# Performance work log

Measured on AMD Instinct MI355X. Metric: run time of the kernel, lower is better.

Reference implementation:

```python
import math
import jax, jax.numpy as jnp
import numpy as np

B, C, D = 4, 1024, 2048
N_EXP, TOP_K, CAP_F = 8, 2, 1.25


def setup_inputs() -> dict:
    key = jax.random.key(0)
    k1, k2, k3, k4 = jax.random.split(key, 4)
    x = jax.random.normal(k1, (B, C, D), dtype=jnp.float32)
    noise = jax.random.normal(k2, (B, C, N_EXP), dtype=jnp.float32)
    w_g = jax.random.normal(k3, (N_EXP, D), dtype=jnp.float32) * 0.02
    w_noise = jax.random.normal(k4, (N_EXP, D), dtype=jnp.float32) * 0.02
    return {"x": x, "noise": noise, "w_g": w_g, "w_noise": w_noise}


def reference(x, noise, w_g, w_noise):
    b, c, d = x.shape
    T = b * c  # num_tokens
    E, k = w_g.shape[0], TOP_K

    # gating logits with noisy top-k (noise eps passed in explicitly)
    logits = jnp.einsum('bcd,ed->bce', x, w_g)
    logits = logits + jax.nn.softplus(jnp.einsum('bcd,ed->bce', x, w_noise)) * noise

    top_vals, top_idx = jax.lax.top_k(logits, k)  # (B,C,k)

    # scatter top-k logits into -inf tensor then softmax == mask non-topk to -inf
    onehot_k = jax.nn.one_hot(top_idx, E, dtype=jnp.int32)  # (B,C,k,E)
    topk_mask = onehot_k.sum(axis=-2) > 0                   # (B,C,E)
    router_probs = jax.nn.softmax(jnp.where(topk_mask, logits, -jnp.inf), axis=-1)

    cap = math.floor(k * CAP_F * T / E)
    cap += cap % 2

    # (k, T, E) expert assignment mask
    exp_mask = onehot_k.reshape(T, k, E).transpose(1, 0, 2)
    # position-in-expert rank via cumulative sum over (k*T, E)
    exp_rank = jnp.cumsum(exp_mask.reshape(k * T, E), axis=0) - 1
    exp_rank = exp_rank.reshape(k, T, E)
    exp_mask = exp_mask * (exp_rank < cap).astype(jnp.int32)
    rank = jnp.sum(exp_mask * exp_rank, axis=-1)  # (k, T) int

    probs_flat = router_probs.reshape(T, E)[None]          # (1,T,E)
    w = exp_mask.astype(x.dtype) * probs_flat              # (k,T,E)
    rank_oh = jax.nn.one_hot(rank, cap, dtype=x.dtype)     # (k,T,cap)
    # combine weights: (T, E, cap)
    exp_weights = jnp.einsum('kte,ktc->tec', w, rank_oh)
    exp_mask_out = exp_weights != 0                        # bool (T,E,cap)

    x_flat = x.reshape(T, d)
    # dense one-hot dispatch matmul: (E, cap, T) @ (T, d)
    expert_batches = jnp.einsum('tec,td->ecd', exp_mask_out.astype(x.dtype), x_flat)
    return exp_weights, exp_mask_out, expert_batches
```

## Files before the change

kernel.cpp:

```cpp
#include <hip/hip_runtime.h>

#define T_TOKENS 4096
#define D_DIM    2048
#define NEXP     8
#define CAP      1280
#define NSLOTS   (NEXP * CAP)

typedef float f32x4 __attribute__((ext_vector_type(4)));

__global__ void gating_kernel(const float* __restrict__ x,
                              const float* __restrict__ noise,
                              const float* __restrict__ w_g,
                              const float* __restrict__ w_noise,
                              int*   __restrict__ top_idx,
                              float* __restrict__ top_prob)
{
    const int wave = threadIdx.x >> 6;
    const int lane = threadIdx.x & 63;
    const int t = blockIdx.x * 4 + wave;
    if (t >= T_TOKENS) return;

    const f32x4* xv = reinterpret_cast<const f32x4*>(x + (size_t)t * D_DIM);

    float acc[16];
#pragma unroll
    for (int j = 0; j < 16; ++j) acc[j] = 0.f;

#pragma unroll
    for (int it = 0; it < 8; ++it) {
        const int c = it * 64 + lane;
        const f32x4 xval = xv[c];
#pragma unroll
        for (int e = 0; e < NEXP; ++e) {
            const f32x4 g = reinterpret_cast<const f32x4*>(w_g + (size_t)e * D_DIM)[c];
            acc[e] += xval.x * g.x + xval.y * g.y + xval.z * g.z + xval.w * g.w;
            const f32x4 n = reinterpret_cast<const f32x4*>(w_noise + (size_t)e * D_DIM)[c];
            acc[8 + e] += xval.x * n.x + xval.y * n.y + xval.z * n.z + xval.w * n.w;
        }
    }

#pragma unroll
    for (int j = 0; j < 16; ++j) {
        float v = acc[j];
#pragma unroll
        for (int off = 32; off > 0; off >>= 1) v += __shfl_down(v, off, 64);
        acc[j] = v;
    }

    if (lane == 0) {
        float logit[NEXP];
#pragma unroll
        for (int e = 0; e < NEXP; ++e) {
            const float z = acc[8 + e];
            const float sp = fmaxf(z, 0.f) + log1pf(expf(-fabsf(z)));
            logit[e] = acc[e] + sp * noise[(size_t)t * NEXP + e];
        }
        int i0 = 0; float v0 = logit[0];
#pragma unroll
        for (int e = 1; e < NEXP; ++e) {
            if (logit[e] > v0) { v0 = logit[e]; i0 = e; }
        }
        int i1 = -1; float v1 = -3.402823466e38f;
#pragma unroll
        for (int e = 0; e < NEXP; ++e) {
            if (e != i0 && logit[e] > v1) { v1 = logit[e]; i1 = e; }
        }
        const float e1  = expf(v1 - v0);
        const float inv = 1.f / (1.f + e1);
        top_idx[t]            = i0;
        top_idx[T_TOKENS + t] = i1;
        top_prob[t]            = inv;
        top_prob[T_TOKENS + t] = e1 * inv;
    }
}

__global__ void scan_kernel(const int* __restrict__ top_idx,
                            int* __restrict__ rank,
                            int* __restrict__ slot_token)
{
    __shared__ int sidx[2 * T_TOKENS];
    __shared__ int scnt[8];

    const int e    = blockIdx.x;
    const int w    = threadIdx.x >> 6;
    const int lane = threadIdx.x & 63;

    for (int i = threadIdx.x; i < 2 * T_TOKENS; i += 512)
        sidx[i] = top_idx[i];
    for (int r = threadIdx.x; r < CAP; r += 512)
        slot_token[e * CAP + r] = -1;
    __syncthreads();

    int cnt = 0;
#pragma unroll
    for (int c = 0; c < 16; ++c) {
        const int i = (w * 16 + c) * 64 + lane;
        cnt += __popcll(__ballot(sidx[i] == e));
    }
    if (lane == 0) scnt[w] = cnt;
    __syncthreads();

    int base = 0;
#pragma unroll
    for (int j = 0; j < 8; ++j) if (j < w) base += scnt[j];

#pragma unroll
    for (int c = 0; c < 16; ++c) {
        const int i = (w * 16 + c) * 64 + lane;
        const bool match = (sidx[i] == e);
        const unsigned long long m = __ballot(match);
        if (match) {
            const int r = base + __popcll(m & ((1ull << lane) - 1ull));
            const bool keep = (r < CAP);
            rank[i] = keep ? r : -1;
            if (keep) slot_token[e * CAP + r] = i;
        }
        base += __popcll(m);
    }
}

__global__ void writer_kernel(const float* __restrict__ x,
                              const int*   __restrict__ top_idx,
                              const float* __restrict__ top_prob,
                              const int*   __restrict__ rank,
                              const int*   __restrict__ slot_token,
                              float* __restrict__ exp_weights,
                              float* __restrict__ exp_mask,
                              float* __restrict__ expert_batches)
{
    const int bid = blockIdx.x;

    if (bid < T_TOKENS) {
        const int t  = bid;
        const int e0 = top_idx[t];
        const int e1 = top_idx[T_TOKENS + t];
        const int r0 = rank[t];
        const int r1 = rank[T_TOKENS + t];
        const float w0 = top_prob[t];
        const float w1 = top_prob[T_TOKENS + t];

        const int p0 = (r0 >= 0) ? (e0 * CAP + r0) : -1;
        const int p1 = (r1 >= 0) ? (e1 * CAP + r1) : -1;
        const float m0 = (w0 != 0.f) ? 1.f : 0.f;
        const float m1 = (w1 != 0.f) ? 1.f : 0.f;

        f32x4* wout = reinterpret_cast<f32x4*>(exp_weights + (size_t)t * NSLOTS);
        f32x4* mout = reinterpret_cast<f32x4*>(exp_mask    + (size_t)t * NSLOTS);

#pragma unroll
        for (int f = threadIdx.x; f < NSLOTS / 4; f += 256) {
            const int b = 4 * f;
            f32x4 wv, mv;
            wv.x = (b     == p0) ? w0 : (b     == p1) ? w1 : 0.f;
            wv.y = (b + 1 == p0) ? w0 : (b + 1 == p1) ? w1 : 0.f;
            wv.z = (b + 2 == p0) ? w0 : (b + 2 == p1) ? w1 : 0.f;
            wv.w = (b + 3 == p0) ? w0 : (b + 3 == p1) ? w1 : 0.f;
            mv.x = (b     == p0) ? m0 : (b     == p1) ? m1 : 0.f;
            mv.y = (b + 1 == p0) ? m0 : (b + 1 == p1) ? m1 : 0.f;
            mv.z = (b + 2 == p0) ? m0 : (b + 2 == p1) ? m1 : 0.f;
            mv.w = (b + 3 == p0) ? m0 : (b + 3 == p1) ? m1 : 0.f;
            __builtin_nontemporal_store(wv, wout + f);
            __builtin_nontemporal_store(mv, mout + f);
        }
    } else {
        const int slot = bid - T_TOKENS;
        const int i = slot_token[slot];
        f32x4* dst = reinterpret_cast<f32x4*>(expert_batches + (size_t)slot * D_DIM);

        if (i >= 0) {
            const int t = i & (T_TOKENS - 1);
            const f32x4* src = reinterpret_cast<const f32x4*>(x + (size_t)t * D_DIM);
#pragma unroll
            for (int c = threadIdx.x; c < D_DIM / 4; c += 256)
                __builtin_nontemporal_store(src[c], dst + c);
        } else {
            const f32x4 z = {0.f, 0.f, 0.f, 0.f};
#pragma unroll
            for (int c = threadIdx.x; c < D_DIM / 4; c += 256)
                __builtin_nontemporal_store(z, dst + c);
        }
    }
}

extern "C" void kernel_launch(void* const* d_in, const int* in_sizes, int n_in,
                              void* d_out, int out_size, void* d_ws, size_t ws_size,
                              hipStream_t stream)
{
    const float* x       = (const float*)d_in[0];
    const float* noise   = (const float*)d_in[1];
    const float* w_g     = (const float*)d_in[2];
    const float* w_noise = (const float*)d_in[3];

    float* out = (float*)d_out;
    const size_t n_ew = (size_t)T_TOKENS * NEXP * CAP;
    float* exp_weights    = out;
    float* exp_mask       = out + n_ew;
    float* expert_batches = out + 2 * n_ew;

    int*   top_idx    = (int*)d_ws;
    float* top_prob   = (float*)((char*)d_ws + 2 * T_TOKENS * 4);
    int*   rank       = (int*)((char*)d_ws + 4 * T_TOKENS * 4);
    int*   slot_token = (int*)((char*)d_ws + 6 * T_TOKENS * 4);

    gating_kernel<<<T_TOKENS / 4, 256, 0, stream>>>(x, noise, w_g, w_noise,
                                                    top_idx, top_prob);
    scan_kernel<<<NEXP, 512, 0, stream>>>(top_idx, rank, slot_token);
    writer_kernel<<<T_TOKENS + NSLOTS, 256, 0, stream>>>(x, top_idx, top_prob,
                                                         rank, slot_token,
                                                         exp_weights, exp_mask,
                                                         expert_batches);
}
```

Baseline: 121.2 us.

## Overlap zero-fill of weight/mask outputs with gating and scatter nonzeros in scan

The dense zero fill of exp_weights and exp_mask moves into extra blocks of the gating kernel, so it runs alongside the gating matmul. The scan kernel then scatters the few nonzero weight and mask entries directly, which removes the per-token writer pass and its compare-and-select work. The final kernel now only copies expert batches. The cost is a stricter ordering: the scatter relies on the fill having finished first, which holds because the kernels run in order on one stream, and the scatter stores are uncoalesced.

Measured after the change: 119.0 us. About the same (-1.8%).

```diff
diff --git a/kernel.cpp b/kernel.cpp
--- a/kernel.cpp
+++ b/kernel.cpp
@@ -6,19 +6,35 @@
 #define CAP      1280
 #define NSLOTS   (NEXP * CAP)
 
+#define GATE_BLOCKS (T_TOKENS / 4)
+#define FILL_FLOATS (2ull * T_TOKENS * NSLOTS)
+#define FILL_VEC_PER_BLOCK 4096
+#define FILL_BLOCKS (FILL_FLOATS / (4 * FILL_VEC_PER_BLOCK))
+
 typedef float f32x4 __attribute__((ext_vector_type(4)));
 
-__global__ void gating_kernel(const float* __restrict__ x,
-                              const float* __restrict__ noise,
-                              const float* __restrict__ w_g,
-                              const float* __restrict__ w_noise,
-                              int*   __restrict__ top_idx,
-                              float* __restrict__ top_prob)
+__global__ void gate_fill_kernel(const float* __restrict__ x,
+                                 const float* __restrict__ noise,
+                                 const float* __restrict__ w_g,
+                                 const float* __restrict__ w_noise,
+                                 int*   __restrict__ top_idx,
+                                 float* __restrict__ top_prob,
+                                 float* __restrict__ wm_base)
 {
+    if (blockIdx.x >= GATE_BLOCKS) {
+        const size_t blk = blockIdx.x - GATE_BLOCKS;
+        f32x4* dst = reinterpret_cast<f32x4*>(wm_base) + blk * FILL_VEC_PER_BLOCK;
+#pragma unroll
+        for (int j = 0; j < FILL_VEC_PER_BLOCK / 256; ++j) {
+            const f32x4 z = {0.f, 0.f, 0.f, 0.f};
+            __builtin_nontemporal_store(z, dst + j * 256 + threadIdx.x);
+        }
+        return;
+    }
+
     const int wave = threadIdx.x >> 6;
     const int lane = threadIdx.x & 63;
     const int t = blockIdx.x * 4 + wave;
-    if (t >= T_TOKENS) return;
 
     const f32x4* xv = reinterpret_cast<const f32x4*>(x + (size_t)t * D_DIM);
 
@@ -74,9 +90,11 @@
     }
 }
 
-__global__ void scan_kernel(const int* __restrict__ top_idx,
-                            int* __restrict__ rank,
-                            int* __restrict__ slot_token)
+__global__ void scan_scatter_kernel(const int*   __restrict__ top_idx,
+                                    const float* __restrict__ top_prob,
+                                    int*   __restrict__ slot_token,
+                                    float* __restrict__ exp_weights,
+                                    float* __restrict__ exp_mask)
 {
     __shared__ int sidx[2 * T_TOKENS];
     __shared__ int scnt[8];
@@ -111,74 +129,38 @@
         const unsigned long long m = __ballot(match);
         if (match) {
             const int r = base + __popcll(m & ((1ull << lane) - 1ull));
-            const bool keep = (r < CAP);
-            rank[i] = keep ? r : -1;
-            if (keep) slot_token[e * CAP + r] = i;
+            if (r < CAP) {
+                slot_token[e * CAP + r] = i;
+                const int t = i & (T_TOKENS - 1);
+                const float wgt = top_prob[i];
+                const size_t off = (size_t)t * NSLOTS + e * CAP + r;
+                exp_weights[off] = wgt;
+                exp_mask[off]    = (wgt != 0.f) ? 1.f : 0.f;
+            }
         }
         base += __popcll(m);
     }
 }
 
-__global__ void writer_kernel(const float* __restrict__ x,
-                              const int*   __restrict__ top_idx,
-                              const float* __restrict__ top_prob,
-                              const int*   __restrict__ rank,
-                              const int*   __restrict__ slot_token,
-                              float* __restrict__ exp_weights,
-                              float* __restrict__ exp_mask,
-                              float* __restrict__ expert_batches)
+__global__ void batches_kernel(const float* __restrict__ x,
+                               const int*   __restrict__ slot_token,
+                               float* __restrict__ expert_batches)
 {
-    const int bid = blockIdx.x;
+    const int slot = blockIdx.x;
+    const int i = slot_token[slot];
+    f32x4* dst = reinterpret_cast<f32x4*>(expert_batches + (size_t)slot * D_DIM);
 
-    if (bid < T_TOKENS) {
-        const int t  = bid;
-        const int e0 = top_idx[t];
-        const int e1 = top_idx[T_TOKENS + t];
-        const int r0 = rank[t];
-        const int r1 = rank[T_TOKENS + t];
-        const float w0 = top_prob[t];
-        const float w1 = top_prob[T_TOKENS + t];
-
-        const int p0 = (r0 >= 0) ? (e0 * CAP + r0) : -1;
-        const int p1 = (r1 >= 0) ? (e1 * CAP + r1) : -1;
-        const float m0 = (w0 != 0.f) ? 1.f : 0.f;
-        const float m1 = (w1 != 0.f) ? 1.f : 0.f;
-
-        f32x4* wout = reinterpret_cast<f32x4*>(exp_weights + (size_t)t * NSLOTS);
-        f32x4* mout = reinterpret_cast<f32x4*>(exp_mask    + (size_t)t * NSLOTS);
-
+    if (i >= 0) {
+        const int t = i & (T_TOKENS - 1);
+        const f32x4* src = reinterpret_cast<const f32x4*>(x + (size_t)t * D_DIM);
 #pragma unroll
-        for (int f = threadIdx.x; f < NSLOTS / 4; f += 256) {
-            const int b = 4 * f;
-            f32x4 wv, mv;
-            wv.x = (b     == p0) ? w0 : (b     == p1) ? w1 : 0.f;
-            wv.y = (b + 1 == p0) ? w0 : (b + 1 == p1) ? w1 : 0.f;
-            wv.z = (b + 2 == p0) ? w0 : (b + 2 == p1) ? w1 : 0.f;
-            wv.w = (b + 3 == p0) ? w0 : (b + 3 == p1) ? w1 : 0.f;
-            mv.x = (b     == p0) ? m0 : (b     == p1) ? m1 : 0.f;
-            mv.y = (b + 1 == p0) ? m0 : (b + 1 == p1) ? m1 : 0.f;
-            mv.z = (b + 2 == p0) ? m0 : (b + 2 == p1) ? m1 : 0.f;
-            mv.w = (b + 3 == p0) ? m0 : (b + 3 == p1) ? m1 : 0.f;
-            __builtin_nontemporal_store(wv, wout + f);
-            __builtin_nontemporal_store(mv, mout + f);
-        }
+        for (int c = threadIdx.x; c < D_DIM / 4; c += 256)
+            __builtin_nontemporal_store(src[c], dst + c);
     } else {
-        const int slot = bid - T_TOKENS;
-        const int i = slot_token[slot];
-        f32x4* dst = reinterpret_cast<f32x4*>(expert_batches + (size_t)slot * D_DIM);
-
-        if (i >= 0) {
-            const int t = i & (T_TOKENS - 1);
-            const f32x4* src = reinterpret_cast<const f32x4*>(x + (size_t)t * D_DIM);
+        const f32x4 z = {0.f, 0.f, 0.f, 0.f};
 #pragma unroll
-            for (int c = threadIdx.x; c < D_DIM / 4; c += 256)
-                __builtin_nontemporal_store(src[c], dst + c);
-        } else {
-            const f32x4 z = {0.f, 0.f, 0.f, 0.f};
-#pragma unroll
-            for (int c = threadIdx.x; c < D_DIM / 4; c += 256)
-                __builtin_nontemporal_store(z, dst + c);
-        }
+        for (int c = threadIdx.x; c < D_DIM / 4; c += 256)
+            __builtin_nontemporal_store(z, dst + c);
     }
 }
 
@@ -199,14 +181,11 @@
 
     int*   top_idx    = (int*)d_ws;
     float* top_prob   = (float*)((char*)d_ws + 2 * T_TOKENS * 4);
-    int*   rank       = (int*)((char*)d_ws + 4 * T_TOKENS * 4);
-    int*   slot_token = (int*)((char*)d_ws + 6 * T_TOKENS * 4);
+    int*   slot_token = (int*)((char*)d_ws + 4 * T_TOKENS * 4);
 
-    gating_kernel<<<T_TOKENS / 4, 256, 0, stream>>>(x, noise, w_g, w_noise,
-                                                    top_idx, top_prob);
-    scan_kernel<<<NEXP, 512, 0, stream>>>(top_idx, rank, slot_token);
-    writer_kernel<<<T_TOKENS + NSLOTS, 256, 0, stream>>>(x, top_idx, top_prob,
-                                                         rank, slot_token,
-                                                         exp_weights, exp_mask,
-                                                         expert_batches);
+    gate_fill_kernel<<<GATE_BLOCKS + FILL_BLOCKS, 256, 0, stream>>>(
+        x, noise, w_g, w_noise, top_idx, top_prob, exp_weights);
+    scan_scatter_kernel<<<NEXP, 512, 0, stream>>>(top_idx, top_prob, slot_token,
+                                                  exp_weights, exp_mask);
+    batches_kernel<<<NSLOTS, 256, 0, stream>>>(x, slot_token, expert_batches);
 }
```
